# Performance work log

Hardware: AMD Instinct MI355X
Metric: run time of the kernel (lower is better)

Reference implementation:

```python
import jax, jax.numpy as jnp
import numpy as np

BN_EPS = 1e-5
NUM_HEADS = 4

def conv1x1_bn_silu(x, w, gamma, beta, mean, var):
    # x: (B,C,H,W), w: (Cout,Cin) -- 1x1 conv, no bias; BN in eval mode; SiLU act
    y = jnp.einsum('bchw,oc->bohw', x, w)
    g = (gamma / jnp.sqrt(var + BN_EPS))[:, None, None]
    b = (beta - mean * gamma / jnp.sqrt(var + BN_EPS))[:, None, None]
    y = y * g + b
    return y * jax.nn.sigmoid(y)

def setup_inputs() -> dict:
    key = jax.random.key(0)
    ks = jax.random.split(key, 16)
    B, H, W, C = 4, 64, 64, 256
    N = H * W
    Ckv = C // 4 * 2  # kv conv out channels = 128
    inp = {
        'x': jax.random.normal(ks[0], (B, N, C), jnp.float32),
        'y': jax.random.normal(ks[1], (B, N, C), jnp.float32),
        'H': H,
        'W': W,
        'q_w': jax.random.normal(ks[2], (C, C), jnp.float32) * (1.0 / np.sqrt(C)),
        'q_gamma': jax.random.uniform(ks[3], (C,), jnp.float32) + 0.5,
        'q_beta': jax.random.normal(ks[4], (C,), jnp.float32) * 0.1,
        'q_mean': jax.random.normal(ks[5], (C,), jnp.float32) * 0.1,
        'q_var': jax.random.uniform(ks[6], (C,), jnp.float32) + 0.5,
        'kv_w': jax.random.normal(ks[7], (Ckv, C), jnp.float32) * (1.0 / np.sqrt(C)),
        'kv_gamma': jax.random.uniform(ks[8], (Ckv,), jnp.float32) + 0.5,
        'kv_beta': jax.random.normal(ks[9], (Ckv,), jnp.float32) * 0.1,
        'kv_mean': jax.random.normal(ks[10], (Ckv,), jnp.float32) * 0.1,
        'kv_var': jax.random.uniform(ks[11], (Ckv,), jnp.float32) + 0.5,
        'proj_w': jax.random.normal(ks[12], (C, C), jnp.float32) * (1.0 / np.sqrt(C)),
        'proj_b': jax.random.normal(ks[13], (C,), jnp.float32) * 0.1,
    }
    return inp

def reference(x, y, H, W, q_w, q_gamma, q_beta, q_mean, q_var,
              kv_w, kv_gamma, kv_beta, kv_mean, kv_var, proj_w, proj_b):
    B, N, C = x.shape
    nh = NUM_HEADS
    hd = C // nh
    scale = hd ** -0.5
    x4 = x.reshape(B, C, H, W)
    y4 = y.reshape(B, C, H, W)
    # q: (B,C,H,W) -> raw reshape (B,N,nh,hd) -> (B,nh,N,hd)  (faithful to torch code)
    q = conv1x1_bn_silu(x4, q_w, q_gamma, q_beta, q_mean, q_var)
    q = q.reshape(B, N, nh, hd).transpose(0, 2, 1, 3)
    # kv: (B,C/2,H,W) -> raw reshape (B,M,2,nh,hd), M = N//4
    kv = conv1x1_bn_silu(y4, kv_w, kv_gamma, kv_beta, kv_mean, kv_var)
    kv = kv.reshape(B, -1, 2, nh, hd).transpose(2, 0, 3, 1, 4)
    k, v = kv[0], kv[1]  # (B,nh,M,hd)
    attn = jnp.einsum('bhnd,bhmd->bhnm', q * scale, k)  # (B,nh,N,M)
    att_map = jax.nn.softmax(attn, axis=-1)
    out = jnp.einsum('bhnm,bhmd->bhnd', att_map, v)  # (B,nh,N,hd)
    out = out.reshape(B, N, C)  # raw reshape, faithful to original
    out = out @ proj_w.T + proj_b
    return out
```

## Files before the change

kernel.cpp:

```cpp
#include <hip/hip_runtime.h>
#include <hip/hip_bf16.h>
#include <math.h>

#define BB 4
#define NTOK 4096
#define CC 256
#define NH 4
#define HD 64
#define CKV 128

typedef _Float16 half8 __attribute__((ext_vector_type(8)));
typedef _Float16 half4 __attribute__((ext_vector_type(4)));
typedef _Float16 half2v __attribute__((ext_vector_type(2)));
typedef float    f32x4 __attribute__((ext_vector_type(4)));
typedef unsigned int uint2v __attribute__((ext_vector_type(2)));
typedef unsigned int uint4v __attribute__((ext_vector_type(4)));

__device__ __forceinline__ unsigned int pkrtz_u(float a, float b) {
  return __builtin_bit_cast(unsigned int, __builtin_amdgcn_cvt_pkrtz(a, b));
}
__device__ __forceinline__ half2v pkrtz(float a, float b) {
  return __builtin_bit_cast(half2v, __builtin_amdgcn_cvt_pkrtz(a, b));
}
__device__ __forceinline__ float exp2_fast(float x) {
  float r;
  asm("v_exp_f32 %0, %1" : "=v"(r) : "v"(x));
  return r;
}
__device__ __forceinline__ int swzi(int row, int d) {
  return row * 64 + (d ^ ((row & 7) << 3));
}
__device__ __forceinline__ int swzv(int row, int d) {
  return row * 64 + (d ^ (((row >> 1) & 7) << 3));
}
__device__ __forceinline__ f32x4 mfma16(half8 a, half8 b, f32x4 c) {
  return __builtin_amdgcn_mfma_f32_16x16x32_f16(a, b, c, 0, 0, 0);
}

__global__ __launch_bounds__(256) void conv_fused(
    const float* __restrict__ x, const float* __restrict__ y,
    const float* __restrict__ qw, const float* __restrict__ qg_, const float* __restrict__ qb,
    const float* __restrict__ qm, const float* __restrict__ qv,
    const float* __restrict__ kw, const float* __restrict__ kg_, const float* __restrict__ kb,
    const float* __restrict__ km, const float* __restrict__ kvv,
    _Float16* __restrict__ qout, _Float16* __restrict__ kvout)
{
  const int ptile = blockIdx.x, oy = blockIdx.y, b = blockIdx.z;
  const bool isq = oy < 4;
  const float* Xsrc = isq ? x : y;
  const float* W    = isq ? qw : kw;
  const float* gam  = isq ? qg_ : kg_;
  const float* bet  = isq ? qb : kb;
  const float* mea  = isq ? qm : km;
  const float* var  = isq ? qv : kvv;
  _Float16*    Yout = isq ? qout : kvout;
  const int otile = isq ? oy : oy - 4;
  const int COUT  = isq ? 256 : 128;

  __shared__ float    T[64 * 132];
  __shared__ _Float16 Xs[128 * 64];
  __shared__ _Float16 Ws[64 * 64];

  const int t = threadIdx.x, wave = t >> 6, lane = t & 63;
  const int lm = lane & 15, lg = lane >> 4;
  const float* Xb = Xsrc + (size_t)b * CC * NTOK + ptile * 128;
  const float* Wb = W + otile * 64 * 256;

  f32x4 acc[2][4];
  #pragma unroll
  for (int m = 0; m < 2; ++m)
    #pragma unroll
    for (int n = 0; n < 4; ++n) acc[m][n] = (f32x4){0.f, 0.f, 0.f, 0.f};

  for (int c0 = 0; c0 < 256; c0 += 64) {
    __syncthreads();
    #pragma unroll
    for (int i = 0; i < 8; ++i) {
      int c = (t >> 5) + i * 8;
      int pcol = (t & 31) * 4;
      *(float4*)&T[c * 132 + pcol] =
          *(const float4*)&Xb[(size_t)(c0 + c) * NTOK + pcol];
    }
    #pragma unroll
    for (int i = 0; i < 2; ++i) {
      int u = t + i * 256; int o = u >> 3, ch = u & 7;
      const float* ws = &Wb[o * 256 + c0 + ch * 8];
      uint4v h;
      #pragma unroll
      for (int j = 0; j < 4; ++j) h[j] = pkrtz_u(ws[j * 2], ws[j * 2 + 1]);
      *(uint4v*)&Ws[swzi(o, ch * 8)] = h;
    }
    __syncthreads();
    {
      int p = t & 127, chh = (t >> 7) * 4;
      #pragma unroll
      for (int cc = 0; cc < 4; ++cc) {
        int ch = chh + cc;
        uint4v h;
        #pragma unroll
        for (int j = 0; j < 4; ++j)
          h[j] = pkrtz_u(T[(ch * 8 + j * 2) * 132 + p], T[(ch * 8 + j * 2 + 1) * 132 + p]);
        *(uint4v*)&Xs[swzi(p, ch * 8)] = h;
      }
    }
    __syncthreads();
    #pragma unroll
    for (int kh = 0; kh < 2; ++kh) {
      half8 af[2], bf[4];
      #pragma unroll
      for (int m = 0; m < 2; ++m) af[m] = *(half8*)&Xs[swzi(wave * 32 + m * 16 + lm, kh * 32 + lg * 8)];
      #pragma unroll
      for (int n = 0; n < 4; ++n) bf[n] = *(half8*)&Ws[swzi(n * 16 + lm, kh * 32 + lg * 8)];
      #pragma unroll
      for (int m = 0; m < 2; ++m)
        #pragma unroll
        for (int n = 0; n < 4; ++n)
          acc[m][n] = mfma16(af[m], bf[n], acc[m][n]);
    }
  }

  float ga[4], bb[4];
  #pragma unroll
  for (int n = 0; n < 4; ++n) {
    int o = otile * 64 + n * 16 + lm;
    float g = gam[o] * rsqrtf(var[o] + 1e-5f);
    ga[n] = g;
    bb[n] = bet[o] - mea[o] * g;
  }
  _Float16* Yb = Yout + (size_t)b * COUT * NTOK;
  #pragma unroll
  for (int m = 0; m < 2; ++m)
    #pragma unroll
    for (int n = 0; n < 4; ++n) {
      int o = otile * 64 + n * 16 + lm;
      float r[4];
      #pragma unroll
      for (int rr = 0; rr < 4; ++rr) {
        float v = acc[m][n][rr] * ga[n] + bb[n];
        r[rr] = v / (1.f + __expf(-v));
      }
      int p = ptile * 128 + wave * 32 + m * 16 + lg * 4;
      *(uint2v*)&Yb[(size_t)o * NTOK + p] =
          (uint2v){pkrtz_u(r[0], r[1]), pkrtz_u(r[2], r[3])};
    }
}

__global__ __launch_bounds__(256) void attn_mfma7(
    const _Float16* __restrict__ Q,
    const _Float16* __restrict__ KV,
    _Float16* __restrict__ O)
{
  const int nt = blockIdx.x, hh = blockIdx.y, b = blockIdx.z;
  const int n0 = nt * 128;
  const int t = threadIdx.x, wave = t >> 6, lane = t & 63;
  const int lm = lane & 15, lg = lane >> 4;
  const int wq = wave * 32;
  const float SCL = 0.125f * 1.44269504f;

  __shared__ _Float16 Kl[2][64 * 64];
  __shared__ _Float16 Vt[2][64 * 64];
  __shared__ _Float16 Pl[128 * 64];

  const _Float16* Qb  = Q  + (size_t)b * (CC * NTOK)  + hh * 64;
  const _Float16* KVb = KV + (size_t)b * (CKV * NTOK) + hh * 64;

  half8 qf[2][2];
  #pragma unroll
  for (int qg = 0; qg < 2; ++qg) {
    int n = n0 + wq + qg * 16 + lm;
    const _Float16* src = Qb + (n >> 4) * 4096 + (n & 15) * 256;
    qf[qg][0] = *(const half8*)(src + lg * 8);
    qf[qg][1] = *(const half8*)(src + 32 + lg * 8);
  }

  half8 ones;
  #pragma unroll
  for (int j = 0; j < 8; ++j) ones[j] = (_Float16)1.f;

  f32x4 acc[2][4], accl[2];
  float m_run[2];
  #pragma unroll
  for (int qg = 0; qg < 2; ++qg) {
    m_run[qg] = -1e30f;
    accl[qg] = (f32x4){0.f, 0.f, 0.f, 0.f};
    #pragma unroll
    for (int dg = 0; dg < 4; ++dg) acc[qg][dg] = (f32x4){0.f, 0.f, 0.f, 0.f};
  }

  const int kkey = t >> 2, kch = (t & 3) * 2;
  const int dvp = (t & 31) * 2, kgv = t >> 5;
  const int koffA = swzi(kkey, kch * 8), koffB = swzi(kkey, kch * 8 + 8);
  const int voffA = swzv(dvp, kgv * 8),  voffB = swzv(dvp + 1, kgv * 8);
  const _Float16* kp = KVb + (size_t)(kkey >> 3) * 4096 + (kkey & 7) * 512 + kch * 8;
  const _Float16* vp = KVb + (size_t)kgv * 4096 + 256 + dvp;

  half8 kreg[2];
  unsigned int vreg[8];

#define PREFETCH() do {                                   \
    kreg[0] = *(const half8*)kp;                          \
    kreg[1] = *(const half8*)(kp + 8);                    \
    _Pragma("unroll")                                     \
    for (int j = 0; j < 8; ++j)                           \
      vreg[j] = *(const unsigned int*)(vp + j * 512);     \
    kp += 8 * 4096; vp += 8 * 4096;                       \
  } while (0)

#define STORE_LDS(buf) do {                               \
    *(half8*)&Kl[buf][koffA] = kreg[0];                   \
    *(half8*)&Kl[buf][koffB] = kreg[1];                   \
    unsigned int l0 = (vreg[0] & 0xffffu) | (vreg[1] << 16);      \
    unsigned int l1 = (vreg[2] & 0xffffu) | (vreg[3] << 16);      \
    unsigned int l2 = (vreg[4] & 0xffffu) | (vreg[5] << 16);      \
    unsigned int l3 = (vreg[6] & 0xffffu) | (vreg[7] << 16);      \
    unsigned int h0 = (vreg[0] >> 16) | (vreg[1] & 0xffff0000u);  \
    unsigned int h1 = (vreg[2] >> 16) | (vreg[3] & 0xffff0000u);  \
    unsigned int h2 = (vreg[4] >> 16) | (vreg[5] & 0xffff0000u);  \
    unsigned int h3 = (vreg[6] >> 16) | (vreg[7] & 0xffff0000u);  \
    *(uint4v*)&Vt[buf][voffA] = (uint4v){l0, l1, l2, l3};         \
    *(uint4v*)&Vt[buf][voffB] = (uint4v){h0, h1, h2, h3};         \
  } while (0)

#define BODY(curb, tt) do {                                            \
    if ((tt) < 15) PREFETCH();                                         \
    f32x4 sc[2][4];                                                    \
    __builtin_amdgcn_s_setprio(1);                                     \
    _Pragma("unroll")                                                  \
    for (int kt = 0; kt < 4; ++kt) {                                   \
      half8 kf0 = *(half8*)&Kl[curb][swzi(kt * 16 + lm, lg * 8)];      \
      half8 kf1 = *(half8*)&Kl[curb][swzi(kt * 16 + lm, 32 + lg * 8)]; \
      _Pragma("unroll")                                                \
      for (int qg = 0; qg < 2; ++qg) {                                 \
        f32x4 z = (f32x4){0.f, 0.f, 0.f, 0.f};                         \
        z = mfma16(kf0, qf[qg][0], z);                                 \
        z = mfma16(kf1, qf[qg][1], z);                                 \
        sc[qg][kt] = z;                                                \
      }                                                                \
    }                                                                  \
    __builtin_amdgcn_s_setprio(0);                                     \
    _Pragma("unroll")                                                  \
    for (int qg = 0; qg < 2; ++qg) {                                   \
      float t0 = fmaxf(fmaxf(sc[qg][0][0], sc[qg][0][1]), sc[qg][0][2]);   \
      float t1 = fmaxf(fmaxf(sc[qg][0][3], sc[qg][1][0]), sc[qg][1][1]);   \
      float t2 = fmaxf(fmaxf(sc[qg][1][2], sc[qg][1][3]), sc[qg][2][0]);   \
      float t3 = fmaxf(fmaxf(sc[qg][2][1], sc[qg][2][2]), sc[qg][2][3]);   \
      float t4 = fmaxf(fmaxf(sc[qg][3][0], sc[qg][3][1]), sc[qg][3][2]);   \
      float tm = fmaxf(fmaxf(fmaxf(t0, t1), t2),                           \
                       fmaxf(fmaxf(t3, t4), sc[qg][3][3]));                \
      tm *= SCL;                                                       \
      tm = fmaxf(tm, __shfl_xor(tm, 16, 64));                          \
      tm = fmaxf(tm, __shfl_xor(tm, 32, 64));                          \
      if (__any(tm > m_run[qg] + 8.0f)) {                              \
        float mnew = fmaxf(m_run[qg], tm);                             \
        float corr = exp2_fast(m_run[qg] - mnew);                      \
        _Pragma("unroll")                                              \
        for (int dg = 0; dg < 4; ++dg) acc[qg][dg] *= corr;            \
        accl[qg] *= corr;                                              \
        m_run[qg] = mnew;                                              \
      }                                                                \
      int qrow = wq + qg * 16 + lm;                                    \
      _Pragma("unroll")                                                \
      for (int kt = 0; kt < 4; ++kt) {                                 \
        float p0 = exp2_fast(fmaf(sc[qg][kt][0], SCL, -m_run[qg]));    \
        float p1 = exp2_fast(fmaf(sc[qg][kt][1], SCL, -m_run[qg]));    \
        float p2 = exp2_fast(fmaf(sc[qg][kt][2], SCL, -m_run[qg]));    \
        float p3 = exp2_fast(fmaf(sc[qg][kt][3], SCL, -m_run[qg]));    \
        *(uint2v*)&Pl[swzi(qrow, kt * 16 + lg * 4)] =                  \
            (uint2v){pkrtz_u(p0, p1), pkrtz_u(p2, p3)};                \
      }                                                                \
    }                                                                  \
    __builtin_amdgcn_s_setprio(1);                                     \
    _Pragma("unroll")                                                  \
    for (int ka = 0; ka < 2; ++ka) {                                   \
      half8 pf[2];                                                     \
      _Pragma("unroll")                                                \
      for (int qg = 0; qg < 2; ++qg) {                                 \
        pf[qg] = *(half8*)&Pl[swzi(wq + qg * 16 + lm, ka * 32 + lg * 8)];  \
        accl[qg] = mfma16(ones, pf[qg], accl[qg]);                     \
      }                                                                \
      _Pragma("unroll")                                                \
      for (int dg = 0; dg < 4; ++dg) {                                 \
        half8 vf = *(half8*)&Vt[curb][swzv(dg * 16 + lm, ka * 32 + lg * 8)]; \
        _Pragma("unroll")                                              \
        for (int qg = 0; qg < 2; ++qg)                                 \
          acc[qg][dg] = mfma16(vf, pf[qg], acc[qg][dg]);               \
      }                                                                \
    }                                                                  \
    __builtin_amdgcn_s_setprio(0);                                     \
    if ((tt) < 15) STORE_LDS(curb ^ 1);                                \
    __syncthreads();                                                   \
  } while (0)

  PREFETCH();
  STORE_LDS(0);
  __syncthreads();

  #pragma unroll 1
  for (int it8 = 0; it8 < 8; ++it8) {
    BODY(0, 2 * it8);
    BODY(1, 2 * it8 + 1);
  }

  #pragma unroll
  for (int qg = 0; qg < 2; ++qg) {
    float inv = 1.f / accl[qg][0];
    int n = n0 + wq + qg * 16 + lm;
    _Float16* dst = O + ((size_t)(b * NH + hh) * NTOK + n) * 64;
    #pragma unroll
    for (int dg = 0; dg < 4; ++dg) {
      *(uint2v*)(dst + dg * 16 + lg * 4) =
          (uint2v){pkrtz_u(acc[qg][dg][0] * inv, acc[qg][dg][1] * inv),
                   pkrtz_u(acc[qg][dg][2] * inv, acc[qg][dg][3] * inv)};
    }
  }
#undef PREFETCH
#undef STORE_LDS
#undef BODY
}

__global__ __launch_bounds__(256) void proj_mfma(
    const _Float16* __restrict__ A, const float* __restrict__ Wp,
    const float* __restrict__ bias, float* __restrict__ Out)
{
  const int rtile = blockIdx.x, ctile = blockIdx.y;
  __shared__ _Float16 As[128 * 64];
  __shared__ _Float16 Ws[64 * 64];
  const int t = threadIdx.x, wave = t >> 6, lane = t & 63;
  const int lm = lane & 15, lg = lane >> 4;
  const _Float16* Ab = A + (size_t)rtile * 128 * 256;
  const float* Wb = Wp + ctile * 64 * 256;
  f32x4 acc[2][4];
  #pragma unroll
  for (int m = 0; m < 2; ++m)
    #pragma unroll
    for (int n = 0; n < 4; ++n) acc[m][n] = (f32x4){0.f, 0.f, 0.f, 0.f};

  for (int c0 = 0; c0 < 256; c0 += 64) {
    __syncthreads();
    #pragma unroll
    for (int i = 0; i < 4; ++i) {
      int u = t + i * 256; int r = u >> 3, ch = u & 7;
      *(half8*)&As[swzi(r, ch * 8)] = *(const half8*)&Ab[(size_t)r * 256 + c0 + ch * 8];
    }
    #pragma unroll
    for (int i = 0; i < 2; ++i) {
      int u = t + i * 256; int o = u >> 3, ch = u & 7;
      const float* ws = &Wb[o * 256 + c0 + ch * 8];
      uint4v h;
      #pragma unroll
      for (int j = 0; j < 4; ++j) h[j] = pkrtz_u(ws[j * 2], ws[j * 2 + 1]);
      *(uint4v*)&Ws[swzi(o, ch * 8)] = h;
    }
    __syncthreads();
    #pragma unroll
    for (int kh = 0; kh < 2; ++kh) {
      half8 af[2], bf[4];
      #pragma unroll
      for (int m = 0; m < 2; ++m) af[m] = *(half8*)&As[swzi(wave * 32 + m * 16 + lm, kh * 32 + lg * 8)];
      #pragma unroll
      for (int n = 0; n < 4; ++n) bf[n] = *(half8*)&Ws[swzi(n * 16 + lm, kh * 32 + lg * 8)];
      #pragma unroll
      for (int m = 0; m < 2; ++m)
        #pragma unroll
        for (int n = 0; n < 4; ++n)
          acc[m][n] = mfma16(af[m], bf[n], acc[m][n]);
    }
  }
  float* Ob = Out + (size_t)rtile * 128 * 256 + ctile * 64;
  #pragma unroll
  for (int n = 0; n < 4; ++n) {
    float bia = bias[ctile * 64 + n * 16 + lm];
    #pragma unroll
    for (int m = 0; m < 2; ++m)
      #pragma unroll
      for (int rr = 0; rr < 4; ++rr)
        Ob[(size_t)(wave * 32 + m * 16 + lg * 4 + rr) * 256 + n * 16 + lm] =
            acc[m][n][rr] + bia;
  }
}

extern "C" void kernel_launch(void* const* d_in, const int* in_sizes, int n_in,
                              void* d_out, int out_size, void* d_ws, size_t ws_size,
                              hipStream_t stream) {
  const float* x        = (const float*)d_in[0];
  const float* y        = (const float*)d_in[1];
  const float* q_w      = (const float*)d_in[4];
  const float* q_gamma  = (const float*)d_in[5];
  const float* q_beta   = (const float*)d_in[6];
  const float* q_mean   = (const float*)d_in[7];
  const float* q_var    = (const float*)d_in[8];
  const float* kv_w     = (const float*)d_in[9];
  const float* kv_gamma = (const float*)d_in[10];
  const float* kv_beta  = (const float*)d_in[11];
  const float* kv_mean  = (const float*)d_in[12];
  const float* kv_var   = (const float*)d_in[13];
  const float* proj_w   = (const float*)d_in[14];
  const float* proj_b   = (const float*)d_in[15];
  float* out = (float*)d_out;

  _Float16* qbn  = (_Float16*)d_ws;
  _Float16* kvbn = qbn  + (size_t)BB * CC * NTOK;
  _Float16* aout = kvbn + (size_t)BB * CKV * NTOK;

  conv_fused<<<dim3(32, 6, BB), 256, 0, stream>>>(
      x, y, q_w, q_gamma, q_beta, q_mean, q_var,
      kv_w, kv_gamma, kv_beta, kv_mean, kv_var, qbn, kvbn);
  attn_mfma7<<<dim3(32, NH, BB), 256, 0, stream>>>(qbn, kvbn, aout);
  proj_mfma<<<dim3(128, 4), 256, 0, stream>>>(aout, proj_w, proj_b, out);
}
```

Measured before the change: 60.60 us.

## Split attention key range in two and merge partials in a combine kernel

The attention kernel now splits the 1024 keys into two halves, each handled by a separate block. Each block writes a normalized partial output plus its running max and sum, and a new combine kernel merges the halves with log-sum-exp rescaling. This doubles the grid from 512 to 1024 blocks to fill the GPU's compute units better. The cost is an extra kernel launch, extra global traffic for the partial outputs, and fp16 rounding of the partials before they are merged.

```diff
diff --git a/kernel.cpp b/kernel.cpp
--- a/kernel.cpp
+++ b/kernel.cpp
@@ -10,7 +10,6 @@
 #define CKV 128
 
 typedef _Float16 half8 __attribute__((ext_vector_type(8)));
-typedef _Float16 half4 __attribute__((ext_vector_type(4)));
 typedef _Float16 half2v __attribute__((ext_vector_type(2)));
 typedef float    f32x4 __attribute__((ext_vector_type(4)));
 typedef unsigned int uint2v __attribute__((ext_vector_type(2)));
@@ -18,9 +17,6 @@
 
 __device__ __forceinline__ unsigned int pkrtz_u(float a, float b) {
   return __builtin_bit_cast(unsigned int, __builtin_amdgcn_cvt_pkrtz(a, b));
-}
-__device__ __forceinline__ half2v pkrtz(float a, float b) {
-  return __builtin_bit_cast(half2v, __builtin_amdgcn_cvt_pkrtz(a, b));
 }
 __device__ __forceinline__ float exp2_fast(float x) {
   float r;
@@ -132,25 +128,29 @@
   for (int m = 0; m < 2; ++m)
     #pragma unroll
     for (int n = 0; n < 4; ++n) {
-      int o = otile * 64 + n * 16 + lm;
       float r[4];
       #pragma unroll
       for (int rr = 0; rr < 4; ++rr) {
         float v = acc[m][n][rr] * ga[n] + bb[n];
         r[rr] = v / (1.f + __expf(-v));
       }
+      int o = otile * 64 + n * 16 + lm;
       int p = ptile * 128 + wave * 32 + m * 16 + lg * 4;
       *(uint2v*)&Yb[(size_t)o * NTOK + p] =
           (uint2v){pkrtz_u(r[0], r[1]), pkrtz_u(r[2], r[3])};
     }
 }
 
-__global__ __launch_bounds__(256) void attn_mfma7(
+__global__ __launch_bounds__(256) void attn_split(
     const _Float16* __restrict__ Q,
     const _Float16* __restrict__ KV,
-    _Float16* __restrict__ O)
+    _Float16* __restrict__ O1,
+    _Float16* __restrict__ O2,
+    float2* __restrict__ LM1,
+    float2* __restrict__ LM2)
 {
-  const int nt = blockIdx.x, hh = blockIdx.y, b = blockIdx.z;
+  const int nt = blockIdx.x, hh = blockIdx.y;
+  const int b = blockIdx.z & (BB - 1), sp = blockIdx.z >> 2;
   const int n0 = nt * 128;
   const int t = threadIdx.x, wave = t >> 6, lane = t & 63;
   const int lm = lane & 15, lg = lane >> 4;
@@ -191,8 +191,10 @@
   const int dvp = (t & 31) * 2, kgv = t >> 5;
   const int koffA = swzi(kkey, kch * 8), koffB = swzi(kkey, kch * 8 + 8);
   const int voffA = swzv(dvp, kgv * 8),  voffB = swzv(dvp + 1, kgv * 8);
-  const _Float16* kp = KVb + (size_t)(kkey >> 3) * 4096 + (kkey & 7) * 512 + kch * 8;
-  const _Float16* vp = KVb + (size_t)kgv * 4096 + 256 + dvp;
+  const _Float16* kp = KVb + (size_t)sp * 64 * 4096
+                     + (size_t)(kkey >> 3) * 4096 + (kkey & 7) * 512 + kch * 8;
+  const _Float16* vp = KVb + (size_t)sp * 64 * 4096
+                     + (size_t)kgv * 4096 + 256 + dvp;
 
   half8 kreg[2];
   unsigned int vreg[8];
@@ -222,7 +224,7 @@
   } while (0)
 
 #define BODY(curb, tt) do {                                            \
-    if ((tt) < 15) PREFETCH();                                         \
+    if ((tt) < 7) PREFETCH();                                          \
     f32x4 sc[2][4];                                                    \
     __builtin_amdgcn_s_setprio(1);                                     \
     _Pragma("unroll")                                                  \
@@ -287,7 +289,7 @@
       }                                                                \
     }                                                                  \
     __builtin_amdgcn_s_setprio(0);                                     \
-    if ((tt) < 15) STORE_LDS(curb ^ 1);                                \
+    if ((tt) < 7) STORE_LDS(curb ^ 1);                                 \
     __syncthreads();                                                   \
   } while (0)
 
@@ -296,16 +298,21 @@
   __syncthreads();
 
   #pragma unroll 1
-  for (int it8 = 0; it8 < 8; ++it8) {
-    BODY(0, 2 * it8);
-    BODY(1, 2 * it8 + 1);
-  }
-
+  for (int it = 0; it < 4; ++it) {
+    BODY(0, 2 * it);
+    BODY(1, 2 * it + 1);
+  }
+
+  _Float16* Opart = sp ? O2 : O1;
+  float2*   LMp   = sp ? LM2 : LM1;
   #pragma unroll
   for (int qg = 0; qg < 2; ++qg) {
-    float inv = 1.f / accl[qg][0];
+    float l = accl[qg][0];
+    float inv = 1.f / l;
     int n = n0 + wq + qg * 16 + lm;
-    _Float16* dst = O + ((size_t)(b * NH + hh) * NTOK + n) * 64;
+    size_t row = (size_t)(b * NH + hh) * NTOK + n;
+    if (lg == 0) LMp[row] = make_float2(m_run[qg], l);
+    _Float16* dst = Opart + row * 64;
     #pragma unroll
     for (int dg = 0; dg < 4; ++dg) {
       *(uint2v*)(dst + dg * 16 + lg * 4) =
@@ -316,6 +323,34 @@
 #undef PREFETCH
 #undef STORE_LDS
 #undef BODY
+}
+
+__global__ __launch_bounds__(256) void attn_combine(
+    const _Float16* __restrict__ O2,
+    const float2* __restrict__ LM1, const float2* __restrict__ LM2,
+    _Float16* __restrict__ O1)
+{
+  int gid = blockIdx.x * 256 + threadIdx.x;
+  int row = gid >> 2, seg = (gid & 3) * 16;
+  float2 lm1 = LM1[row], lm2 = LM2[row];
+  float m = fmaxf(lm1.x, lm2.x);
+  float a1 = lm1.y * exp2_fast(lm1.x - m);
+  float a2 = lm2.y * exp2_fast(lm2.x - m);
+  float inv = 1.f / (a1 + a2);
+  float c1 = a1 * inv, c2 = a2 * inv;
+  _Float16* p1 = O1 + (size_t)row * 64 + seg;
+  const _Float16* p2 = O2 + (size_t)row * 64 + seg;
+  #pragma unroll
+  for (int h = 0; h < 2; ++h) {
+    half8 o1 = *(half8*)(p1 + h * 8);
+    half8 o2 = *(const half8*)(p2 + h * 8);
+    uint4v r;
+    #pragma unroll
+    for (int j = 0; j < 4; ++j)
+      r[j] = pkrtz_u((float)o1[j * 2]     * c1 + (float)o2[j * 2]     * c2,
+                     (float)o1[j * 2 + 1] * c1 + (float)o2[j * 2 + 1] * c2);
+    *(uint4v*)(p1 + h * 8) = r;
+  }
 }
 
 __global__ __launch_bounds__(256) void proj_mfma(
@@ -398,13 +433,19 @@
   const float* proj_b   = (const float*)d_in[15];
   float* out = (float*)d_out;
 
+  const size_t NROWS = (size_t)BB * NH * NTOK;
   _Float16* qbn  = (_Float16*)d_ws;
   _Float16* kvbn = qbn  + (size_t)BB * CC * NTOK;
-  _Float16* aout = kvbn + (size_t)BB * CKV * NTOK;
+  _Float16* o1   = kvbn + (size_t)BB * CKV * NTOK;
+  _Float16* o2   = o1   + NROWS * HD;
+  float2*   lm1  = (float2*)(o2 + NROWS * HD);
+  float2*   lm2  = lm1 + NROWS;
 
   conv_fused<<<dim3(32, 6, BB), 256, 0, stream>>>(
       x, y, q_w, q_gamma, q_beta, q_mean, q_var,
       kv_w, kv_gamma, kv_beta, kv_mean, kv_var, qbn, kvbn);
-  attn_mfma7<<<dim3(32, NH, BB), 256, 0, stream>>>(qbn, kvbn, aout);
-  proj_mfma<<<dim3(128, 4), 256, 0, stream>>>(aout, proj_w, proj_b, out);
-}
+  attn_split<<<dim3(32, NH, BB * 2), 256, 0, stream>>>(
+      qbn, kvbn, o1, o2, lm1, lm2);
+  attn_combine<<<1024, 256, 0, stream>>>(o2, lm1, lm2, o1);
+  proj_mfma<<<dim3(128, 4), 256, 0, stream>>>(o1, proj_w, proj_b, out);
+}
```

After: 68.75 us. 13.4% more time.
